# Performance work log

Measured on AMD Instinct MI355X. Metric: run time of the kernel, lower is better.

Reference implementation:

```python
import jax, jax.numpy as jnp
import numpy as np

N_NODES = 100000
N_EDGES = 1600000
N_PAIRS = 200000
IN_CH = 128
HID_CH = 128


def _graph_conv(x, src, dst, edge_weight, w_rel, b_rel, w_root, num_nodes):
    # PyG GraphConv with aggr='mean':
    # out = lin_rel(mean_{j in N(i)}(x_j * w_ij)) + lin_root(x_i)
    msg = x[src] * edge_weight[:, None]                       # [E, C] gather
    agg = jax.ops.segment_sum(msg, dst, num_segments=num_nodes)  # [N, C]
    cnt = jax.ops.segment_sum(jnp.ones((src.shape[0],), x.dtype), dst,
                              num_segments=num_nodes)          # in-degree
    agg = agg / jnp.maximum(cnt, 1.0)[:, None]                 # mean aggr
    return agg @ w_rel + b_rel + x @ w_root


def setup_inputs() -> dict:
    key = jax.random.key(0)
    ks = jax.random.split(key, 10)
    x = jax.random.normal(ks[0], (N_NODES, IN_CH), dtype=jnp.float32)
    edge_index = jax.random.randint(ks[1], (2, N_EDGES), 0, N_NODES, dtype=jnp.int32)
    edge_weight = jax.random.uniform(ks[2], (N_EDGES,), dtype=jnp.float32)
    edge_label_index = jax.random.randint(ks[3], (2, N_PAIRS), 0, N_NODES, dtype=jnp.int32)
    s1 = 1.0 / np.sqrt(IN_CH)
    s2 = 1.0 / np.sqrt(HID_CH)
    w1_rel = jax.random.uniform(ks[4], (IN_CH, HID_CH), jnp.float32, -s1, s1)
    b1_rel = jnp.zeros((HID_CH,), jnp.float32)
    w1_root = jax.random.uniform(ks[5], (IN_CH, HID_CH), jnp.float32, -s1, s1)
    w2_rel = jax.random.uniform(ks[6], (HID_CH, HID_CH), jnp.float32, -s2, s2)
    b2_rel = jnp.zeros((HID_CH,), jnp.float32)
    w2_root = jax.random.uniform(ks[7], (HID_CH, HID_CH), jnp.float32, -s2, s2)
    return {"x": x, "edge_index": edge_index, "edge_weight": edge_weight,
            "edge_label_index": edge_label_index,
            "w1_rel": w1_rel, "b1_rel": b1_rel, "w1_root": w1_root,
            "w2_rel": w2_rel, "b2_rel": b2_rel, "w2_root": w2_root}


def reference(x, edge_index, edge_weight, edge_label_index,
              w1_rel, b1_rel, w1_root, w2_rel, b2_rel, w2_root):
    src, dst = edge_index[0], edge_index[1]
    # encode
    h = _graph_conv(x, src, dst, edge_weight, w1_rel, b1_rel, w1_root, x.shape[0])
    h = jax.nn.relu(h)
    z = _graph_conv(h, src, dst, edge_weight, w2_rel, b2_rel, w2_root, x.shape[0])
    # decode: scaled dot product between candidate pair embeddings
    zs = z[edge_label_index[0]]   # [P, H]
    zd = z[edge_label_index[1]]   # [P, H]
    scale = z.shape[-1] ** 0.5
    return jnp.sum(zs * zd, axis=-1) / scale
```

## Files before the change

kernel.cpp:

```cpp
#include <hip/hip_runtime.h>

#define NN 100000
#define NE 1600000
#define NP 200000
#define CH 128
#define LK 264

#define BSH 6
#define NB  1563
#define G1  256
#define EPB (NE / G1)
#define CAP3 4096

typedef _Float16 f16x8 __attribute__((ext_vector_type(8)));
typedef _Float16 f16x2 __attribute__((ext_vector_type(2)));
typedef float f32x4 __attribute__((ext_vector_type(4)));

__global__ void cast_kernel(const float* __restrict__ in, _Float16* __restrict__ out, int n8) {
    int i = blockIdx.x * blockDim.x + threadIdx.x;
    if (i >= n8) return;
    const float4* p = (const float4*)in + (size_t)i * 2;
    float4 a = p[0], b = p[1];
    f16x8 o = { (_Float16)a.x, (_Float16)a.y, (_Float16)a.z, (_Float16)a.w,
                (_Float16)b.x, (_Float16)b.y, (_Float16)b.z, (_Float16)b.w };
    *((f16x8*)out + i) = o;
}

__global__ __launch_bounds__(256)
void bucket_hist_kernel(const int* __restrict__ dst, int* __restrict__ hist ) {
    __shared__ int s_h[NB];
    for (int i = threadIdx.x; i < NB; i += 256) s_h[i] = 0;
    __syncthreads();
    int start = blockIdx.x * EPB, end = start + EPB;
    for (int e = start + threadIdx.x; e < end; e += 256)
        atomicAdd(&s_h[dst[e] >> BSH], 1);
    __syncthreads();
    int* row = hist + (size_t)blockIdx.x * NB;
    for (int i = threadIdx.x; i < NB; i += 256) row[i] = s_h[i];
}

__global__ void colscan_kernel(int* __restrict__ hist, int* __restrict__ totals) {
    int b = blockIdx.x * blockDim.x + threadIdx.x;
    if (b >= NB) return;
    int run = 0;
    for (int g = 0; g < G1; g++) {
        size_t idx = (size_t)g * NB + b;
        int v = hist[idx];
        hist[idx] = run;
        run += v;
    }
    totals[b] = run;
}

__global__ __launch_bounds__(1024)
void scanB_kernel(const int* __restrict__ totals, int* __restrict__ base) {
    __shared__ int s[2048];
    int tid = threadIdx.x;
    for (int i = tid; i < 2048; i += 1024) s[i] = (i < NB) ? totals[i] : 0;
    __syncthreads();
    for (int off = 1; off < 2048; off <<= 1) {
        int i0 = tid, i1 = tid + 1024;
        int v0 = (i0 >= off) ? s[i0 - off] : 0;
        int v1 = (i1 >= off) ? s[i1 - off] : 0;
        __syncthreads();
        s[i0] += v0; s[i1] += v1;
        __syncthreads();
    }
    if (tid == 0) base[0] = 0;
    for (int i = tid; i < NB; i += 1024) base[i + 1] = s[i];
}

__global__ __launch_bounds__(256)
void bucket_scatter_kernel(const int* __restrict__ src, const int* __restrict__ dst,
                           const float* __restrict__ ew, const int* __restrict__ hist,
                           const int* __restrict__ base, int2* __restrict__ tmp) {
    __shared__ int s_cur[NB];
    const int* row = hist + (size_t)blockIdx.x * NB;
    for (int i = threadIdx.x; i < NB; i += 256) s_cur[i] = base[i] + row[i];
    __syncthreads();
    int start = blockIdx.x * EPB, end = start + EPB;
    for (int e = start + threadIdx.x; e < end; e += 256) {
        int d = dst[e];
        int b = d >> BSH;
        int pos = atomicAdd(&s_cur[b], 1);
        tmp[pos] = make_int2(src[e] | ((d & 63) << 17), __float_as_int(ew[e]));
    }
}

__global__ __launch_bounds__(256)
void bucket_finalize_kernel(const int2* __restrict__ tmp, const int* __restrict__ base,
                            int* __restrict__ row_ptr, int2* __restrict__ csr, int N) {
    __shared__ int2 s_e[CAP3];
    __shared__ int s_cnt[64], s_off[64];
    int b = blockIdx.x;
    int lo = base[b], hi = base[b + 1];
    int size = hi - lo;
    int nbase = b << BSH;
    int ncnt = min(64, N - nbase);
    int tid = threadIdx.x;
    if (tid < 64) s_cnt[tid] = 0;
    bool inlds = (size <= CAP3);
    __syncthreads();
    if (inlds) {
        for (int i = tid; i < size; i += 256) {
            int2 e = tmp[lo + i];
            s_e[i] = e;
            atomicAdd(&s_cnt[(e.x >> 17) & 63], 1);
        }
    } else {
        for (int i = tid; i < size; i += 256) {
            int2 e = tmp[lo + i];
            atomicAdd(&s_cnt[(e.x >> 17) & 63], 1);
        }
    }
    __syncthreads();
    if (tid == 0) {
        int run = 0;
        for (int i = 0; i < 64; i++) { int v = s_cnt[i]; s_off[i] = run; s_cnt[i] = run; run += v; }
    }
    __syncthreads();
    if (tid < ncnt) row_ptr[nbase + tid] = lo + s_off[tid];
    if (b == NB - 1 && tid == 0) row_ptr[N] = hi;
    if (inlds) {
        for (int i = tid; i < size; i += 256) {
            int2 e = s_e[i];
            int dl = (e.x >> 17) & 63;
            int p = atomicAdd(&s_cnt[dl], 1);
            csr[lo + p] = make_int2(e.x & 0x1FFFF, e.y);
        }
    } else {
        for (int i = tid; i < size; i += 256) {
            int2 e = tmp[lo + i];
            int dl = (e.x >> 17) & 63;
            int p = atomicAdd(&s_cnt[dl], 1);
            csr[lo + p] = make_int2(e.x & 0x1FFFF, e.y);
        }
    }
}

__global__ __launch_bounds__(256)
void gather_kernel(const _Float16* __restrict__ feat, const int* __restrict__ row_ptr,
                   const int2* __restrict__ csr, _Float16* __restrict__ agg, int N) {
    int node = blockIdx.x * 4 + (threadIdx.x >> 6);
    if (node >= N) return;
    int lane = threadIdx.x & 63;
    int q = lane >> 4;
    int l16 = lane & 15;
    int c8 = l16 << 3;
    int r0 = row_ptr[node], r1 = row_ptr[node + 1];
    float acc[8] = {0.f, 0.f, 0.f, 0.f, 0.f, 0.f, 0.f, 0.f};
    int r = r0 + q;
    if (r < r1) {
        int2 e = csr[r];
        f16x8 v = *(const f16x8*)&feat[(size_t)e.x * CH + c8];
        for (r += 4; r < r1; r += 4) {
            int2 e2 = csr[r];
            f16x8 v2 = *(const f16x8*)&feat[(size_t)e2.x * CH + c8];
            float w = __int_as_float(e.y);
#pragma unroll
            for (int j = 0; j < 8; j++) acc[j] += w * (float)v[j];
            e = e2; v = v2;
        }
        float w = __int_as_float(e.y);
#pragma unroll
        for (int j = 0; j < 8; j++) acc[j] += w * (float)v[j];
    }
#pragma unroll
    for (int j = 0; j < 8; j++) {
        acc[j] += __shfl_xor(acc[j], 16, 64);
        acc[j] += __shfl_xor(acc[j], 32, 64);
    }
    if (q == 0) {
        float inv = 1.0f / fmaxf((float)(r1 - r0), 1.0f);
        f16x8 o;
#pragma unroll
        for (int j = 0; j < 8; j++) o[j] = (_Float16)(acc[j] * inv);
        *(f16x8*)&agg[(size_t)node * CH + c8] = o;
    }
}

__global__ void prep_w_kernel(const float* __restrict__ wr, const float* __restrict__ wo,
                              _Float16* __restrict__ wt) {
    int idx = blockIdx.x * 256 + threadIdx.x;
    if (idx >= 128 * 256) return;
    int n = idx >> 8, k = idx & 255;
    float v = (k < 128) ? wr[k * 128 + n] : wo[(k - 128) * 128 + n];
    wt[idx] = (_Float16)v;
}

template <bool RELU>
__global__ __launch_bounds__(256)
void layer_mfma_kernel(const _Float16* __restrict__ agg,
                       const _Float16* __restrict__ xin,
                       const _Float16* __restrict__ wt,
                       const float* __restrict__ bias,
                       _Float16* __restrict__ out, int N) {
    __shared__ _Float16 s_a[64][LK];

    const int tid = threadIdx.x;
    const int nb = blockIdx.x * 64;

    for (int i = tid; i < 64 * 32; i += 256) {
        int r = i >> 5;
        int c8 = (i & 31) << 3;
        int gn = nb + r;
        f16x8 v = {};
        if (gn < N) {
            const _Float16* srcp = (c8 < 128) ? &agg[(size_t)gn * CH + c8]
                                              : &xin[(size_t)gn * CH + (c8 - 128)];
            v = *(const f16x8*)srcp;
        }
        *(f16x8*)&s_a[r][c8] = v;
    }
    __syncthreads();

    const int wave = tid >> 6;
    const int lane = tid & 63;
    const int quad = lane >> 4;
    const int l16  = lane & 15;

    f32x4 acc[4][2];
#pragma unroll
    for (int m = 0; m < 4; m++)
#pragma unroll
        for (int t = 0; t < 2; t++) acc[m][t] = (f32x4){0.f, 0.f, 0.f, 0.f};

    const int kq = quad * 8;

#pragma unroll
    for (int ks = 0; ks < 8; ks++) {
        int kbase = ks * 32 + kq;
        f16x8 bf[2];
#pragma unroll
        for (int t = 0; t < 2; t++) {
            int n = wave * 32 + t * 16 + l16;
            bf[t] = *(const f16x8*)&wt[(size_t)n * 256 + kbase];
        }
#pragma unroll
        for (int m = 0; m < 4; m++) {
            f16x8 af = *(const f16x8*)&s_a[m * 16 + l16][kbase];
            acc[m][0] = __builtin_amdgcn_mfma_f32_16x16x32_f16(af, bf[0], acc[m][0], 0, 0, 0);
            acc[m][1] = __builtin_amdgcn_mfma_f32_16x16x32_f16(af, bf[1], acc[m][1], 0, 0, 0);
        }
    }

    float bv[2];
    bv[0] = bias[wave * 32 + l16];
    bv[1] = bias[wave * 32 + 16 + l16];

#pragma unroll
    for (int m = 0; m < 4; m++) {
#pragma unroll
        for (int r = 0; r < 4; r++) {
            int node = nb + m * 16 + quad * 4 + r;
            if (node >= N) continue;
#pragma unroll
            for (int t = 0; t < 2; t++) {
                float v = acc[m][t][r] + bv[t];
                if (RELU) v = fmaxf(v, 0.f);
                out[(size_t)node * CH + wave * 32 + t * 16 + l16] = (_Float16)v;
            }
        }
    }
}

__global__ void decode_kernel(const _Float16* __restrict__ z,
                              const int* __restrict__ ps,
                              const int* __restrict__ pd,
                              float* __restrict__ out, int P) {
    long tid = (long)blockIdx.x * blockDim.x + threadIdx.x;
    int p = (int)(tid >> 6);
    int lane = (int)(tid & 63);
    if (p >= P) return;
    int s = ps[p], d = pd[p];
    f16x2 a = *(const f16x2*)&z[(size_t)s * CH + lane * 2];
    f16x2 b = *(const f16x2*)&z[(size_t)d * CH + lane * 2];
    float v = (float)a[0] * (float)b[0] + (float)a[1] * (float)b[1];
#pragma unroll
    for (int off = 32; off > 0; off >>= 1) v += __shfl_down(v, off, 64);
    if (lane == 0) out[p] = v * 0.08838834764831845f;
}

extern "C" void kernel_launch(void* const* d_in, const int* in_sizes, int n_in,
                              void* d_out, int out_size, void* d_ws, size_t ws_size,
                              hipStream_t stream) {
    const float* x       = (const float*)d_in[0];
    const int*   ei      = (const int*)d_in[1];
    const float* ew      = (const float*)d_in[2];
    const int*   eli     = (const int*)d_in[3];
    const float* w1_rel  = (const float*)d_in[4];
    const float* b1      = (const float*)d_in[5];
    const float* w1_root = (const float*)d_in[6];
    const float* w2_rel  = (const float*)d_in[7];
    const float* b2      = (const float*)d_in[8];
    const float* w2_root = (const float*)d_in[9];
    float* out = (float*)d_out;

    const int N = NN, E = NE, P = NP;
    const size_t hrow = (size_t)N * CH * sizeof(_Float16);

    char* ws = (char*)d_ws;
    size_t off = 0;
    auto alloc = [&](size_t bytes) { char* p = ws + off; off = (off + bytes + 15) & ~(size_t)15; return p; };
    _Float16* xh   = (_Float16*)alloc(hrow);
    _Float16* aggh = (_Float16*)alloc(hrow);
    _Float16* hh   = (_Float16*)alloc(hrow);
    _Float16* zh   = aggh;
    int* hist     = (int*)alloc((size_t)G1 * NB * 4);
    int* totals   = (int*)alloc((size_t)NB * 4);
    int* base     = (int*)alloc((size_t)(NB + 1) * 4);
    int* row_ptr  = (int*)alloc((size_t)(N + 1) * 4);
    int2* tmp     = (int2*)alloc((size_t)E * 8);
    int2* csr     = (int2*)alloc((size_t)E * 8);
    _Float16* w1t = (_Float16*)alloc((size_t)128 * 256 * 2);
    _Float16* w2t = (_Float16*)alloc((size_t)128 * 256 * 2);

    const int* src = ei;
    const int* dst = ei + E;

    const int n8 = N * CH / 8;

    cast_kernel<<<(n8 + 255) / 256, 256, 0, stream>>>(x, xh, n8);
    prep_w_kernel<<<128, 256, 0, stream>>>(w1_rel, w1_root, w1t);
    prep_w_kernel<<<128, 256, 0, stream>>>(w2_rel, w2_root, w2t);

    bucket_hist_kernel<<<G1, 256, 0, stream>>>(dst, hist);
    colscan_kernel<<<(NB + 255) / 256, 256, 0, stream>>>(hist, totals);
    scanB_kernel<<<1, 1024, 0, stream>>>(totals, base);
    bucket_scatter_kernel<<<G1, 256, 0, stream>>>(src, dst, ew, hist, base, tmp);
    bucket_finalize_kernel<<<NB, 256, 0, stream>>>(tmp, base, row_ptr, csr, N);

    gather_kernel<<<(N + 3) / 4, 256, 0, stream>>>(xh, row_ptr, csr, aggh, N);
    layer_mfma_kernel<true><<<(N + 63) / 64, 256, 0, stream>>>(aggh, xh, w1t, b1, hh, N);

    gather_kernel<<<(N + 3) / 4, 256, 0, stream>>>(hh, row_ptr, csr, aggh, N);
    layer_mfma_kernel<false><<<(N + 63) / 64, 256, 0, stream>>>(aggh, hh, w2t, b2, zh, N);

    {
        long threads = (long)P * 64;
        decode_kernel<<<(int)((threads + 255) / 256), 256, 0, stream>>>(zh, eli, eli + P, out, P);
    }
}
```

Before: 410.3 us.

## Parallelize column scan with wave scans, merge weight prep, widen decode loads

```diff
diff --git a/kernel.cpp b/kernel.cpp
--- a/kernel.cpp
+++ b/kernel.cpp
@@ -13,7 +13,7 @@
 #define CAP3 4096
 
 typedef _Float16 f16x8 __attribute__((ext_vector_type(8)));
-typedef _Float16 f16x2 __attribute__((ext_vector_type(2)));
+typedef _Float16 f16x4 __attribute__((ext_vector_type(4)));
 typedef float f32x4 __attribute__((ext_vector_type(4)));
 
 __global__ void cast_kernel(const float* __restrict__ in, _Float16* __restrict__ out, int n8) {
@@ -39,17 +39,29 @@
     for (int i = threadIdx.x; i < NB; i += 256) row[i] = s_h[i];
 }
 
-__global__ void colscan_kernel(int* __restrict__ hist, int* __restrict__ totals) {
-    int b = blockIdx.x * blockDim.x + threadIdx.x;
+__global__ __launch_bounds__(256)
+void colscan_kernel(int* __restrict__ hist, int* __restrict__ totals) {
+    int b = blockIdx.x * 4 + (threadIdx.x >> 6);
     if (b >= NB) return;
-    int run = 0;
-    for (int g = 0; g < G1; g++) {
-        size_t idx = (size_t)g * NB + b;
-        int v = hist[idx];
-        hist[idx] = run;
-        run += v;
-    }
-    totals[b] = run;
+    int lane = threadIdx.x & 63;
+    size_t base = (size_t)(lane * 4) * NB + b;
+    int v0 = hist[base];
+    int v1 = hist[base + NB];
+    int v2 = hist[base + 2 * (size_t)NB];
+    int v3 = hist[base + 3 * (size_t)NB];
+    int s0 = v0, s1 = s0 + v1, s2 = s1 + v2, s3 = s2 + v3;
+    int incl = s3;
+#pragma unroll
+    for (int off = 1; off < 64; off <<= 1) {
+        int n = __shfl_up(incl, off, 64);
+        if (lane >= off) incl += n;
+    }
+    int excl = incl - s3;
+    hist[base] = excl;
+    hist[base + NB] = excl + s0;
+    hist[base + 2 * (size_t)NB] = excl + s1;
+    hist[base + 3 * (size_t)NB] = excl + s2;
+    if (lane == 63) totals[b] = incl;
 }
 
 __global__ __launch_bounds__(1024)
@@ -179,13 +191,19 @@
     }
 }
 
-__global__ void prep_w_kernel(const float* __restrict__ wr, const float* __restrict__ wo,
-                              _Float16* __restrict__ wt) {
+__global__ void prep_w2_kernel(const float* __restrict__ w1r, const float* __restrict__ w1o,
+                               const float* __restrict__ w2r, const float* __restrict__ w2o,
+                               _Float16* __restrict__ w1t, _Float16* __restrict__ w2t) {
     int idx = blockIdx.x * 256 + threadIdx.x;
-    if (idx >= 128 * 256) return;
-    int n = idx >> 8, k = idx & 255;
+    if (idx >= 2 * 128 * 256) return;
+    int which = idx >> 15;
+    int li = idx & 32767;
+    int n = li >> 8, k = li & 255;
+    const float* wr = which ? w2r : w1r;
+    const float* wo = which ? w2o : w1o;
+    _Float16* wt = which ? w2t : w1t;
     float v = (k < 128) ? wr[k * 128 + n] : wo[(k - 128) * 128 + n];
-    wt[idx] = (_Float16)v;
+    wt[li] = (_Float16)v;
 }
 
 template <bool RELU>
@@ -269,15 +287,16 @@
                               const int* __restrict__ pd,
                               float* __restrict__ out, int P) {
     long tid = (long)blockIdx.x * blockDim.x + threadIdx.x;
-    int p = (int)(tid >> 6);
-    int lane = (int)(tid & 63);
+    int p = (int)(tid >> 5);
+    int lane = (int)(tid & 31);
     if (p >= P) return;
     int s = ps[p], d = pd[p];
-    f16x2 a = *(const f16x2*)&z[(size_t)s * CH + lane * 2];
-    f16x2 b = *(const f16x2*)&z[(size_t)d * CH + lane * 2];
-    float v = (float)a[0] * (float)b[0] + (float)a[1] * (float)b[1];
-#pragma unroll
-    for (int off = 32; off > 0; off >>= 1) v += __shfl_down(v, off, 64);
+    f16x4 a = *(const f16x4*)&z[(size_t)s * CH + lane * 4];
+    f16x4 b = *(const f16x4*)&z[(size_t)d * CH + lane * 4];
+    float v = (float)a[0] * (float)b[0] + (float)a[1] * (float)b[1]
+            + (float)a[2] * (float)b[2] + (float)a[3] * (float)b[3];
+#pragma unroll
+    for (int off = 16; off > 0; off >>= 1) v += __shfl_xor(v, off, 64);
     if (lane == 0) out[p] = v * 0.08838834764831845f;
 }
 
@@ -321,11 +340,10 @@
     const int n8 = N * CH / 8;
 
     cast_kernel<<<(n8 + 255) / 256, 256, 0, stream>>>(x, xh, n8);
-    prep_w_kernel<<<128, 256, 0, stream>>>(w1_rel, w1_root, w1t);
-    prep_w_kernel<<<128, 256, 0, stream>>>(w2_rel, w2_root, w2t);
+    prep_w2_kernel<<<256, 256, 0, stream>>>(w1_rel, w1_root, w2_rel, w2_root, w1t, w2t);
 
     bucket_hist_kernel<<<G1, 256, 0, stream>>>(dst, hist);
-    colscan_kernel<<<(NB + 255) / 256, 256, 0, stream>>>(hist, totals);
+    colscan_kernel<<<(NB + 3) / 4, 256, 0, stream>>>(hist, totals);
     scanB_kernel<<<1, 1024, 0, stream>>>(totals, base);
     bucket_scatter_kernel<<<G1, 256, 0, stream>>>(src, dst, ew, hist, base, tmp);
     bucket_finalize_kernel<<<NB, 256, 0, stream>>>(tmp, base, row_ptr, csr, N);
@@ -337,7 +355,7 @@
     layer_mfma_kernel<false><<<(N + 63) / 64, 256, 0, stream>>>(aggh, hh, w2t, b2, zh, N);
 
     {
-        long threads = (long)P * 64;
+        long threads = (long)P * 32;
         decode_kernel<<<(int)((threads + 255) / 256), 256, 0, stream>>>(zh, eli, eli + P, out, P);
     }
 }
```

Measured after the change: 387.4 us. 1.06x faster.
